# Performance work log

Measured on AMD Instinct MI355X. Metric: run time of the kernel, lower is better.

The kernel has to match this reference:

```python
import jax, jax.numpy as jnp
import numpy as np

N = 100_000   # nodes
E = 1_600_000 # edges per graph
D = 64        # feature width
HA = 32       # attention hidden


def setup_inputs() -> dict:
    key = jax.random.key(0)
    ks = jax.random.split(key, 20)
    inp = {}
    inp["h"] = jax.random.normal(ks[0], (N, D), jnp.float32)
    inp["e_od"] = jax.random.normal(ks[1], (E, D), jnp.float32)
    inp["e_ad"] = jax.random.normal(ks[2], (E, D), jnp.float32)
    inp["src_od"] = jax.random.randint(ks[3], (E,), 0, N)
    inp["dst_od"] = jax.random.randint(ks[4], (E,), 0, N)
    inp["src_ad"] = jax.random.randint(ks[5], (E,), 0, N)
    inp["dst_ad"] = jax.random.randint(ks[6], (E,), 0, N)
    s = 1.0 / np.sqrt(D).astype(np.float32)
    # stacked params: index 0 = OD graph, index 1 = AD graph
    inp["W_src"]  = jax.random.normal(ks[7],  (2, D, D), jnp.float32) * s
    inp["W_dst"]  = jax.random.normal(ks[8],  (2, D, D), jnp.float32) * s
    inp["W_edge"] = jax.random.normal(ks[9],  (2, D, D), jnp.float32) * s
    inp["b_msg"]  = jnp.zeros((2, D), jnp.float32)
    inp["W_self"] = jax.random.normal(ks[10], (2, D, D), jnp.float32) * s
    inp["W_agg"]  = jax.random.normal(ks[11], (2, D, D), jnp.float32) * s
    inp["b_node"] = jnp.zeros((2, D), jnp.float32)
    # Attention (Aggregate_samedim): Linear(D->HA, bias) -> tanh -> Linear(HA->1, no bias)
    inp["attn_l1_w"] = jax.random.normal(ks[12], (D, HA), jnp.float32) * s
    inp["attn_l1_b"] = jnp.zeros((HA,), jnp.float32)
    inp["attn_l2_w"] = jax.random.normal(ks[13], (HA, 1), jnp.float32) * (1.0 / np.sqrt(HA).astype(np.float32))
    return inp


def reference(h, e_od, e_ad, src_od, dst_od, src_ad, dst_ad,
              W_src, W_dst, W_edge, b_msg, W_self, W_agg, b_node,
              attn_l1_w, attn_l1_b, attn_l2_w):
    def mpnn(i, e, src, dst):
        # edge message: gather src/dst node feats, small GEMMs, relu  [E, D]
        m = jax.nn.relu(h[src] @ W_src[i] + h[dst] @ W_dst[i] + e @ W_edge[i] + b_msg[i])
        # scatter-sum to destination nodes  [N, D]
        agg = jax.ops.segment_sum(m, dst, num_segments=N)
        # node update  [N, D]
        return jax.nn.relu(h @ W_self[i] + agg @ W_agg[i] + b_node[i])

    intra = mpnn(0, e_od, src_od, dst_od)  # OD graph node states
    inter = mpnn(1, e_ad, src_ad, dst_ad)  # AD graph node states
    # Aggregate_samedim: attention over the 2-way stack
    rep = jnp.stack([intra, inter], axis=1)               # [N, 2, D]
    w = jnp.tanh(rep @ attn_l1_w + attn_l1_b) @ attn_l2_w  # [N, 2, 1]
    beta = jax.nn.softmax(w, axis=1)
    return (beta * rep).sum(axis=1)                        # [N, D]
```

## Files before the change

### kernel.cpp

```cpp
#include <hip/hip_runtime.h>
#include <hip/hip_bf16.h>

using short8  = __attribute__((ext_vector_type(8))) short;
using ushort8 = __attribute__((ext_vector_type(8))) unsigned short;
using f32x4   = __attribute__((ext_vector_type(4))) float;
using fvec4   = __attribute__((ext_vector_type(4))) float;

#define CH 8192

__device__ inline unsigned short f2bf(float x) {
  union { __hip_bfloat16 b; unsigned short u; } c;
  c.b = __float2bfloat16(x);
  return c.u;
}
__device__ inline float bf2f(unsigned short s) {
  return __uint_as_float(((unsigned int)s) << 16);
}
__device__ inline unsigned int pk2(float lo, float hi) {
  union { __hip_bfloat162 b; unsigned int u; } c;
  c.b = __float22bfloat162_rn(make_float2(lo, hi));
  return c.u;
}
__device__ inline short8 cvt8(fvec4 a, fvec4 b) {
  union { short8 s; unsigned int u[4]; } r;
  r.u[0] = pk2(a[0], a[1]);
  r.u[1] = pk2(a[2], a[3]);
  r.u[2] = pk2(b[0], b[1]);
  r.u[3] = pk2(b[2], b[3]);
  return r.s;
}

__device__ inline void gload_lds16(const void* g, void* l) {
  __builtin_amdgcn_global_load_lds(
      (const __attribute__((address_space(1))) void*)g,
      (__attribute__((address_space(3))) void*)l, 16, 0, 0);
}

__device__ inline void load_bfrags_f32(const float* __restrict__ W, short8 bfr[2][4], int lane) {
  int l15 = lane & 15, lh = lane >> 4;
#pragma unroll
  for (int ks = 0; ks < 2; ++ks)
#pragma unroll
    for (int ct = 0; ct < 4; ++ct) {
      short8 v;
#pragma unroll
      for (int i = 0; i < 8; ++i)
        v[i] = (short)f2bf(W[(ks * 32 + lh * 8 + i) * 64 + ct * 16 + l15]);
      bfr[ks][ct] = v;
    }
}

__device__ inline void load_bfrags(const unsigned short* __restrict__ Wf, short8 bfr[2][4], int lane) {
#pragma unroll
  for (int ks = 0; ks < 2; ++ks)
#pragma unroll
    for (int ct = 0; ct < 4; ++ct) {
      union { ushort8 u; short8 s; } c;
      c.u = *reinterpret_cast<const ushort8*>(Wf + (((ks * 4 + ct) << 9) + (lane << 3)));
      bfr[ks][ct] = c.s;
    }
}

struct PrepArgs {
  const float* W[10];
};

__global__ __launch_bounds__(64) void prep_w_kernel(PrepArgs pw, unsigned short* __restrict__ Wf) {
  int z = blockIdx.x;
  int lane = threadIdx.x & 63;
  short8 bfr[2][4];
  load_bfrags_f32(pw.W[z], bfr, lane);
  unsigned short* dst = Wf + (size_t)z * 4096;
#pragma unroll
  for (int ks = 0; ks < 2; ++ks)
#pragma unroll
    for (int ct = 0; ct < 4; ++ct) {
      union { short8 s; ushort8 u; } c;
      c.s = bfr[ks][ct];
      *reinterpret_cast<ushort8*>(dst + (((ks * 4 + ct) << 9) + (lane << 3))) = c.u;
    }
}

struct ProjArgs {
  unsigned short* out[6];
};

__global__ __launch_bounds__(256) void proj_all_kernel(const float* __restrict__ h,
                                                       const unsigned short* __restrict__ Wf,
                                                       ProjArgs pa, int N) {
  int lane = threadIdx.x & 63;
  int wv = threadIdx.x >> 6;
  int rowbase = blockIdx.x * 256 + wv * 64;
  int l15 = lane & 15, lh = lane >> 4;

  short8 afr[4][2];
#pragma unroll
  for (int rt = 0; rt < 4; ++rt) {
    int row = rowbase + rt * 16 + l15;
    int rc = row < N ? row : 0;
    const fvec4* p = reinterpret_cast<const fvec4*>(h + (size_t)rc * 64);
#pragma unroll
    for (int ks = 0; ks < 2; ++ks)
      afr[rt][ks] = cvt8(p[ks * 8 + lh * 2], p[ks * 8 + lh * 2 + 1]);
  }

  for (int z = 0; z < 6; ++z) {
    short8 bfr[2][4];
    load_bfrags(Wf + (size_t)z * 4096, bfr, lane);
    unsigned short* __restrict__ out = pa.out[z];

    f32x4 acc[4][4];
#pragma unroll
    for (int rt = 0; rt < 4; ++rt)
#pragma unroll
      for (int ct = 0; ct < 4; ++ct) acc[rt][ct] = (f32x4){0.f, 0.f, 0.f, 0.f};

#pragma unroll
    for (int rt = 0; rt < 4; ++rt)
#pragma unroll
      for (int ks = 0; ks < 2; ++ks)
#pragma unroll
        for (int ct = 0; ct < 4; ++ct)
          acc[rt][ct] = __builtin_amdgcn_mfma_f32_16x16x32_bf16(afr[rt][ks], bfr[ks][ct], acc[rt][ct], 0, 0, 0);

#pragma unroll
    for (int rt = 0; rt < 4; ++rt)
#pragma unroll
      for (int rg = 0; rg < 4; ++rg) {
        int row = rowbase + rt * 16 + lh * 4 + rg;
        if (row < N) {
#pragma unroll
          for (int ct = 0; ct < 4; ++ct)
            out[(size_t)row * 64 + ct * 16 + l15] = f2bf(acc[rt][ct][rg]);
        }
      }
  }
}

__global__ __launch_bounds__(256) void hist_kernel(const int* __restrict__ dst0, const int* __restrict__ dst1,
                                                   int* __restrict__ counts, int E, int NBK) {
  __shared__ int hcnt[2048];
  int z = blockIdx.y;
  const int* __restrict__ dst = z ? dst1 : dst0;
  int t = threadIdx.x;
  for (int i = t; i < NBK; i += 256) hcnt[i] = 0;
  __syncthreads();
  int base = blockIdx.x * CH;
#pragma unroll 4
  for (int k = 0; k < CH / 256; ++k) {
    int i = base + k * 256 + t;
    if (i < E) atomicAdd(&hcnt[dst[i] >> 6], 1);
  }
  __syncthreads();
  for (int i = t; i < NBK; i += 256) {
    int c = hcnt[i];
    if (c) atomicAdd(&counts[(size_t)z * NBK + i], c);
  }
}

__global__ __launch_bounds__(1024) void scan_kernel(const int* __restrict__ counts, int* __restrict__ cursor,
                                                    int* __restrict__ gcur, int NBK) {
  int z = blockIdx.x;
  const int* c = counts + (size_t)z * NBK;
  __shared__ int lds[1024];
  int t = threadIdx.x;
  int carry = 0;
  for (int base = 0; base < NBK; base += 1024) {
    int i = base + t;
    int v = (i < NBK) ? c[i] : 0;
    lds[t] = v;
    __syncthreads();
    for (int off = 1; off < 1024; off <<= 1) {
      int x = (t >= off) ? lds[t - off] : 0;
      __syncthreads();
      lds[t] += x;
      __syncthreads();
    }
    if (i < NBK) {
      int excl = carry + lds[t] - v;
      cursor[(size_t)z * NBK + i] = excl;
      gcur[(size_t)z * NBK + i] = excl;
    }
    carry += lds[1023];
    __syncthreads();
  }
}

__global__ __launch_bounds__(256) void scatterA_kernel(
    const int* __restrict__ src0, const int* __restrict__ dst0,
    const int* __restrict__ src1, const int* __restrict__ dst1,
    int* __restrict__ gcur, int2* __restrict__ recs0, int2* __restrict__ recs1,
    int E, int NBK) {
  __shared__ int lcnt[2048];
  int z = blockIdx.y;
  const int* __restrict__ src = z ? src1 : src0;
  const int* __restrict__ dst = z ? dst1 : dst0;
  int2* __restrict__ recs = z ? recs1 : recs0;
  int t = threadIdx.x;
  for (int i = t; i < NBK; i += 256) lcnt[i] = 0;
  __syncthreads();
  int base = blockIdx.x * CH;
#pragma unroll 4
  for (int k = 0; k < CH / 256; ++k) {
    int i = base + k * 256 + t;
    if (i < E) atomicAdd(&lcnt[dst[i] >> 6], 1);
  }
  __syncthreads();
  for (int i = t; i < NBK; i += 256) {
    int c = lcnt[i];
    lcnt[i] = c ? atomicAdd(&gcur[(size_t)z * NBK + i], c) : 0;
  }
  __syncthreads();
#pragma unroll 4
  for (int k = 0; k < CH / 256; ++k) {
    int i = base + k * 256 + t;
    if (i < E) {
      int d = dst[i], s = src[i];
      int bin = d >> 6, dl = d & 63;
      int pos = atomicAdd(&lcnt[bin], 1);
      recs[pos] = make_int2(i | (bin << 21), s | (dl << 26));
    }
  }
}

__global__ __launch_bounds__(256) void sortB_kernel(int2* __restrict__ recs0, int2* __restrict__ recs1,
                                                    const int* __restrict__ cursor,
                                                    const int* __restrict__ counts, int NBK) {
  __shared__ int cnt_lds[64];
  __shared__ int cur_lds[64];
  int z = blockIdx.y;
  int b = blockIdx.x;
  int2* __restrict__ recs = z ? recs1 : recs0;
  int start = cursor[(size_t)z * NBK + b];
  int cnt = counts[(size_t)z * NBK + b];
  int t = threadIdx.x;

  for (int cbase = 0; cbase < cnt; cbase += 2048) {
    int ccnt = min(2048, cnt - cbase);
    int2 r[8];
    int dl[8];
    if (t < 64) cnt_lds[t] = 0;
    __syncthreads();
#pragma unroll
    for (int k = 0; k < 8; ++k) {
      int idx = k * 256 + t;
      if (idx < ccnt) {
        r[k] = recs[start + cbase + idx];
        dl[k] = ((unsigned)r[k].y) >> 26;
        atomicAdd(&cnt_lds[dl[k]], 1);
      }
    }
    __syncthreads();
    if (t < 64) {
      int c = cnt_lds[t];
      int x = c;
#pragma unroll
      for (int off = 1; off < 64; off <<= 1) {
        int y = __shfl_up(x, off);
        if (t >= off) x += y;
      }
      cur_lds[t] = x - c;
    }
    __syncthreads();
#pragma unroll
    for (int k = 0; k < 8; ++k) {
      int idx = k * 256 + t;
      if (idx < ccnt) {
        int pos = atomicAdd(&cur_lds[dl[k]], 1);
        recs[start + cbase + pos] = r[k];
      }
    }
    __syncthreads();
  }
}

struct EdgeArgs {
  const float* e[2];
  const int2* recs[2];
  const unsigned short* We[2];
  const float* bmsg[2];
  const unsigned short* Ps[2];
  const unsigned short* Pd[2];
  float* agg[2];
};

__global__ __launch_bounds__(256) void edge_sorted_kernel(EdgeArgs ea, int E) {
  __shared__ float e_lds[4][64 * 64];

  int z = blockIdx.y;
  const float* __restrict__ e = ea.e[z];
  const int2* __restrict__ recs = ea.recs[z];
  const unsigned short* __restrict__ Psrc = ea.Ps[z];
  const unsigned short* __restrict__ Pdst = ea.Pd[z];
  float* __restrict__ agg = ea.agg[z];

  int lane = threadIdx.x & 63;
  int wv = threadIdx.x >> 6;
  int base = (blockIdx.x * 4 + wv) * 64;
  if (base >= E) return;
  int l15 = lane & 15, lh = lane >> 4;
  char* lbase = (char*)&e_lds[wv][0];

  int slot = base + lane;
  int el = 0, sl = 0, dl = 0;
  if (slot < E) {
    int2 rc = recs[slot];
    el = rc.x & 0x1FFFFF;
    sl = rc.y & 0x3FFFFFF;
    dl = (((rc.x >> 21) & 0x7FF) << 6) | (int)(((unsigned)rc.y) >> 26);
  }

  const float* bmsg = ea.bmsg[z];
  float bv[4];
#pragma unroll
  for (int ct = 0; ct < 4; ++ct) bv[ct] = bmsg[ct * 16 + l15];

  short8 bfr[2][4];
  load_bfrags(ea.We[z], bfr, lane);

  ushort8 aP[8], aD[8];
#pragma unroll
  for (int rt = 0; rt < 4; ++rt) {
    int sr = rt * 16 + l15;
    int hr = __shfl(sl, sr);
    int dr = __shfl(dl, sr);
    const ushort8* ps = reinterpret_cast<const ushort8*>(Psrc + ((size_t)hr << 6));
    const ushort8* pd = reinterpret_cast<const ushort8*>(Pdst + ((size_t)dr << 6));
    aP[rt * 2] = ps[lh];
    aP[rt * 2 + 1] = ps[4 + lh];
    aD[rt * 2] = pd[lh];
    aD[rt * 2 + 1] = pd[4 + lh];
  }
  __builtin_amdgcn_sched_barrier(0);

  int rgrp = lane >> 4;
#pragma unroll
  for (int i = 0; i < 16; ++i) {
    int r = i * 4 + rgrp;
    int er = __shfl(el, r);
    int c = (lane & 15) ^ (r & 7);
    gload_lds16(e + ((size_t)er << 6) + c * 4, lbase + i * 1024);
  }
  __builtin_amdgcn_sched_barrier(0);

  short8 idf[2];
#pragma unroll
  for (int half = 0; half < 2; ++half) {
    short8 v;
#pragma unroll
    for (int i = 0; i < 8; ++i)
      v[i] = (short)((lh * 8 + i == half * 16 + l15) ? 0x3F80 : 0);
    idf[half] = v;
  }

  f32x4 acc[4][4];
#pragma unroll
  for (int ct = 0; ct < 4; ++ct) {
    f32x4 bb = (f32x4){bv[ct], bv[ct], bv[ct], bv[ct]};
#pragma unroll
    for (int rt = 0; rt < 4; ++rt) acc[rt][ct] = bb;
  }

#pragma unroll
  for (int rt = 0; rt < 4; ++rt) {
    union { ushort8 u; short8 s; } aP0, aP1, aD0, aD1;
    aP0.u = aP[rt * 2];
    aP1.u = aP[rt * 2 + 1];
    aD0.u = aD[rt * 2];
    aD1.u = aD[rt * 2 + 1];
    acc[rt][0] = __builtin_amdgcn_mfma_f32_16x16x32_bf16(aP0.s, idf[0], acc[rt][0], 0, 0, 0);
    acc[rt][1] = __builtin_amdgcn_mfma_f32_16x16x32_bf16(aP0.s, idf[1], acc[rt][1], 0, 0, 0);
    acc[rt][2] = __builtin_amdgcn_mfma_f32_16x16x32_bf16(aP1.s, idf[0], acc[rt][2], 0, 0, 0);
    acc[rt][3] = __builtin_amdgcn_mfma_f32_16x16x32_bf16(aP1.s, idf[1], acc[rt][3], 0, 0, 0);
    acc[rt][0] = __builtin_amdgcn_mfma_f32_16x16x32_bf16(aD0.s, idf[0], acc[rt][0], 0, 0, 0);
    acc[rt][1] = __builtin_amdgcn_mfma_f32_16x16x32_bf16(aD0.s, idf[1], acc[rt][1], 0, 0, 0);
    acc[rt][2] = __builtin_amdgcn_mfma_f32_16x16x32_bf16(aD1.s, idf[0], acc[rt][2], 0, 0, 0);
    acc[rt][3] = __builtin_amdgcn_mfma_f32_16x16x32_bf16(aD1.s, idf[1], acc[rt][3], 0, 0, 0);
  }

  asm volatile("s_waitcnt vmcnt(0)" ::: "memory");
  __builtin_amdgcn_sched_barrier(0);

#pragma unroll
  for (int rt = 0; rt < 4; ++rt) {
    int r = rt * 16 + l15;
    int rowbyte = r << 8;
    int x = (r & 7) << 4;
    fvec4 p0 = *reinterpret_cast<const fvec4*>(lbase + rowbyte + (((lh * 2) << 4) ^ x));
    fvec4 p1 = *reinterpret_cast<const fvec4*>(lbase + rowbyte + (((lh * 2 + 1) << 4) ^ x));
    fvec4 p2 = *reinterpret_cast<const fvec4*>(lbase + rowbyte + (((8 + lh * 2) << 4) ^ x));
    fvec4 p3 = *reinterpret_cast<const fvec4*>(lbase + rowbyte + (((9 + lh * 2) << 4) ^ x));
    short8 aE0 = cvt8(p0, p1);
    short8 aE1 = cvt8(p2, p3);
#pragma unroll
    for (int ct = 0; ct < 4; ++ct) {
      acc[rt][ct] = __builtin_amdgcn_mfma_f32_16x16x32_bf16(aE0, bfr[0][ct], acc[rt][ct], 0, 0, 0);
      acc[rt][ct] = __builtin_amdgcn_mfma_f32_16x16x32_bf16(aE1, bfr[1][ct], acc[rt][ct], 0, 0, 0);
    }
  }

#pragma unroll
  for (int rt = 0; rt < 4; ++rt)
#pragma unroll
    for (int ct = 0; ct < 4; ++ct)
#pragma unroll
      for (int rg = 0; rg < 4; ++rg)
        acc[rt][ct][rg] = fmaxf(acc[rt][ct][rg], 0.f);

  int dprev = __shfl_up(dl, 1);
  unsigned long long bnd = __ballot(lane > 0 && dl != dprev);
  int vrows = min(64, E - base);

  int r0 = 0;
  while (r0 < vrows) {
    unsigned long long rest = (r0 < 63) ? (bnd >> (r0 + 1)) : 0ull;
    int r1 = rest ? (r0 + 1 + __builtin_ctzll(rest)) : 64;
    if (r1 > vrows) r1 = vrows;
    int dcur = __shfl(dl, r0);

    float s0 = 0.f, s1 = 0.f, s2 = 0.f, s3 = 0.f;
#pragma unroll
    for (int rt = 0; rt < 4; ++rt) {
      int rs = rt * 16;
      if (r0 <= rs && r1 >= rs + 16) {
#pragma unroll
        for (int rg = 0; rg < 4; ++rg) {
          s0 += acc[rt][0][rg];
          s1 += acc[rt][1][rg];
          s2 += acc[rt][2][rg];
          s3 += acc[rt][3][rg];
        }
      } else if (r0 < rs + 16 && r1 > rs) {
#pragma unroll
        for (int rg = 0; rg < 4; ++rg) {
          int row = rs + lh * 4 + rg;
          bool in = (row >= r0) && (row < r1);
          s0 += in ? acc[rt][0][rg] : 0.f;
          s1 += in ? acc[rt][1][rg] : 0.f;
          s2 += in ? acc[rt][2][rg] : 0.f;
          s3 += in ? acc[rt][3][rg] : 0.f;
        }
      }
    }
    s0 += __shfl_xor(s0, 16); s0 += __shfl_xor(s0, 32);
    s1 += __shfl_xor(s1, 16); s1 += __shfl_xor(s1, 32);
    s2 += __shfl_xor(s2, 16); s2 += __shfl_xor(s2, 32);
    s3 += __shfl_xor(s3, 16); s3 += __shfl_xor(s3, 32);
    float mine = (lh == 0) ? s0 : (lh == 1) ? s1 : (lh == 2) ? s2 : s3;
    atomicAdd(&agg[(size_t)dcur * 64 + lane], mine);
    r0 = r1;
  }
}

struct NodeArgs {
  const float* agg[2];
  const unsigned short* T[2];
  const float* bn[2];
  unsigned short* U[2];
};

__global__ __launch_bounds__(256) void node_kernel(const unsigned short* __restrict__ Wf,
                                                   NodeArgs na, int N) {
  int z = blockIdx.y;
  const float* __restrict__ agg = na.agg[z];
  const unsigned short* __restrict__ T = na.T[z];
  const float* __restrict__ bn = na.bn[z];
  unsigned short* __restrict__ U = na.U[z];
  int lane = threadIdx.x & 63;
  int wv = threadIdx.x >> 6;
  int rowbase = blockIdx.x * 256 + wv * 64;
  int l15 = lane & 15, lh = lane >> 4;

  short8 bfr[2][4];
  load_bfrags(Wf + (size_t)(8 + z) * 4096, bfr, lane);

  f32x4 acc[4][4];
#pragma unroll
  for (int rt = 0; rt < 4; ++rt)
#pragma unroll
    for (int ct = 0; ct < 4; ++ct) acc[rt][ct] = (f32x4){0.f, 0.f, 0.f, 0.f};

#pragma unroll
  for (int rt = 0; rt < 4; ++rt) {
    int row = rowbase + rt * 16 + l15;
    int rc = row < N ? row : 0;
    const fvec4* p = reinterpret_cast<const fvec4*>(agg + (size_t)rc * 64);
#pragma unroll
    for (int ks = 0; ks < 2; ++ks) {
      fvec4 p0 = p[ks * 8 + lh * 2], p1 = p[ks * 8 + lh * 2 + 1];
      short8 ahi = cvt8(p0, p1);
      fvec4 q0, q1;
#pragma unroll
      for (int i = 0; i < 4; ++i) {
        q0[i] = p0[i] - bf2f((unsigned short)ahi[i]);
        q1[i] = p1[i] - bf2f((unsigned short)ahi[i + 4]);
      }
      short8 alo = cvt8(q0, q1);
#pragma unroll
      for (int ct = 0; ct < 4; ++ct) {
        acc[rt][ct] = __builtin_amdgcn_mfma_f32_16x16x32_bf16(ahi, bfr[ks][ct], acc[rt][ct], 0, 0, 0);
        acc[rt][ct] = __builtin_amdgcn_mfma_f32_16x16x32_bf16(alo, bfr[ks][ct], acc[rt][ct], 0, 0, 0);
      }
    }
  }

  float bv[4];
#pragma unroll
  for (int ct = 0; ct < 4; ++ct) bv[ct] = bn[ct * 16 + l15];

#pragma unroll
  for (int rt = 0; rt < 4; ++rt)
#pragma unroll
    for (int rg = 0; rg < 4; ++rg) {
      int row = rowbase + rt * 16 + lh * 4 + rg;
      if (row < N) {
#pragma unroll
        for (int ct = 0; ct < 4; ++ct) {
          int c = ct * 16 + l15;
          float v = acc[rt][ct][rg] + bf2f(T[(size_t)row * 64 + c]) + bv[ct];
          U[(size_t)row * 64 + c] = f2bf(fmaxf(v, 0.0f));
        }
      }
    }
}

__global__ __launch_bounds__(256) void attn_kernel(
    const unsigned short* __restrict__ U0, const unsigned short* __restrict__ U1,
    const float* __restrict__ l1w, const float* __restrict__ l1b, const float* __restrict__ l2w,
    float* __restrict__ out, int N) {
  int t = threadIdx.x;
  int node = blockIdx.x * 64 + (t >> 2);
  int q = t & 3;
  if (node >= N) return;
  size_t b0 = (size_t)node * 64;

  float a0[8], a1[8];
#pragma unroll
  for (int i = 0; i < 8; ++i) { a0[i] = l1b[q * 8 + i]; a1[i] = a0[i]; }

  for (int k = 0; k < 64; ++k) {
    float u0 = bf2f(U0[b0 + k]);
    float u1 = bf2f(U1[b0 + k]);
#pragma unroll
    for (int i = 0; i < 8; ++i) {
      float w = l1w[k * 32 + q * 8 + i];
      a0[i] += u0 * w;
      a1[i] += u1 * w;
    }
  }
  float w0 = 0.f, w1 = 0.f;
#pragma unroll
  for (int i = 0; i < 8; ++i) {
    float l2 = l2w[q * 8 + i];
    w0 += tanhf(a0[i]) * l2;
    w1 += tanhf(a1[i]) * l2;
  }
  w0 += __shfl_xor(w0, 1, 4); w0 += __shfl_xor(w0, 2, 4);
  w1 += __shfl_xor(w1, 1, 4); w1 += __shfl_xor(w1, 2, 4);

  float m = fmaxf(w0, w1);
  float e0 = expf(w0 - m), e1 = expf(w1 - m);
  float inv = 1.0f / (e0 + e1);
  float be0 = e0 * inv, be1 = e1 * inv;

#pragma unroll
  for (int j = 0; j < 16; ++j) {
    int c = q * 16 + j;
    out[b0 + c] = be0 * bf2f(U0[b0 + c]) + be1 * bf2f(U1[b0 + c]);
  }
}

static inline size_t au(size_t x) { return (x + 255) & ~(size_t)255; }

extern "C" void kernel_launch(void* const* d_in, const int* in_sizes, int n_in,
                              void* d_out, int out_size, void* d_ws, size_t ws_size,
                              hipStream_t stream) {
  const float* h      = (const float*)d_in[0];
  const float* e_od   = (const float*)d_in[1];
  const float* e_ad   = (const float*)d_in[2];
  const int* src_od   = (const int*)d_in[3];
  const int* dst_od   = (const int*)d_in[4];
  const int* src_ad   = (const int*)d_in[5];
  const int* dst_ad   = (const int*)d_in[6];
  const float* W_src  = (const float*)d_in[7];
  const float* W_dst  = (const float*)d_in[8];
  const float* W_edge = (const float*)d_in[9];
  const float* b_msg  = (const float*)d_in[10];
  const float* W_self = (const float*)d_in[11];
  const float* W_agg  = (const float*)d_in[12];
  const float* b_node = (const float*)d_in[13];
  const float* l1w    = (const float*)d_in[14];
  const float* l1b    = (const float*)d_in[15];
  const float* l2w    = (const float*)d_in[16];
  float* out = (float*)d_out;

  int N = in_sizes[0] / 64;
  int E = in_sizes[1] / 64;
  int NBK = (N + 63) >> 6;

  char* ws = (char*)d_ws;
  size_t off = 0;
  int* counts = (int*)(ws + off);   off += au((size_t)2 * NBK * sizeof(int));
  float* agg0 = (float*)(ws + off); off += (size_t)N * 64 * sizeof(float);
  float* agg1 = (float*)(ws + off); off += (size_t)N * 64 * sizeof(float);
  size_t zero_bytes = off;
  int* cursor = (int*)(ws + off);   off += au((size_t)2 * NBK * sizeof(int));
  int* gcur   = (int*)(ws + off);   off += au((size_t)2 * NBK * sizeof(int));
  int2* recs0 = (int2*)(ws + off);  off += au((size_t)E * sizeof(int2));
  int2* recs1 = (int2*)(ws + off);  off += au((size_t)E * sizeof(int2));
  unsigned short* Wf = (unsigned short*)(ws + off); off += au((size_t)10 * 4096 * sizeof(unsigned short));
  size_t NP = au((size_t)N * 64 * sizeof(unsigned short));
  unsigned short* Psrc0 = (unsigned short*)(ws + off); off += NP;
  unsigned short* Pdst0 = (unsigned short*)(ws + off); off += NP;
  unsigned short* Psrc1 = (unsigned short*)(ws + off); off += NP;
  unsigned short* Pdst1 = (unsigned short*)(ws + off); off += NP;
  unsigned short* T0    = (unsigned short*)(ws + off); off += NP;
  unsigned short* T1    = (unsigned short*)(ws + off); off += NP;
  unsigned short* U0 = Psrc0;
  unsigned short* U1 = Psrc1;

  hipMemsetAsync(ws, 0, zero_bytes, stream);

  PrepArgs pw;
  pw.W[0] = W_src;         pw.W[1] = W_dst;
  pw.W[2] = W_src + 4096;  pw.W[3] = W_dst + 4096;
  pw.W[4] = W_self;        pw.W[5] = W_self + 4096;
  pw.W[6] = W_edge;        pw.W[7] = W_edge + 4096;
  pw.W[8] = W_agg;         pw.W[9] = W_agg + 4096;
  prep_w_kernel<<<10, 64, 0, stream>>>(pw, Wf);

  int nb = (N + 255) / 256;
  ProjArgs pa;
  pa.out[0] = Psrc0;
  pa.out[1] = Pdst0;
  pa.out[2] = Psrc1;
  pa.out[3] = Pdst1;
  pa.out[4] = T0;
  pa.out[5] = T1;
  proj_all_kernel<<<nb, 256, 0, stream>>>(h, Wf, pa, N);

  int nch = (E + CH - 1) / CH;
  hist_kernel<<<dim3(nch, 2), 256, 0, stream>>>(dst_od, dst_ad, counts, E, NBK);
  scan_kernel<<<2, 1024, 0, stream>>>(counts, cursor, gcur, NBK);
  scatterA_kernel<<<dim3(nch, 2), 256, 0, stream>>>(src_od, dst_od, src_ad, dst_ad, gcur,
                                                    recs0, recs1, E, NBK);
  sortB_kernel<<<dim3(NBK, 2), 256, 0, stream>>>(recs0, recs1, cursor, counts, NBK);

  int tiles = (E + 63) / 64;
  int eb = (tiles + 3) / 4;
  EdgeArgs ea;
  ea.e[0] = e_od;  ea.recs[0] = recs0; ea.We[0] = Wf + 6 * 4096; ea.bmsg[0] = b_msg;
  ea.Ps[0] = Psrc0; ea.Pd[0] = Pdst0; ea.agg[0] = agg0;
  ea.e[1] = e_ad;  ea.recs[1] = recs1; ea.We[1] = Wf + 7 * 4096; ea.bmsg[1] = b_msg + 64;
  ea.Ps[1] = Psrc1; ea.Pd[1] = Pdst1; ea.agg[1] = agg1;
  edge_sorted_kernel<<<dim3(eb, 2), 256, 0, stream>>>(ea, E);

  NodeArgs na;
  na.agg[0] = agg0; na.T[0] = T0; na.bn[0] = b_node;      na.U[0] = U0;
  na.agg[1] = agg1; na.T[1] = T1; na.bn[1] = b_node + 64; na.U[1] = U1;
  node_kernel<<<dim3(nb, 2), 256, 0, stream>>>(Wf, na, N);

  attn_kernel<<<(N + 63) / 64, 256, 0, stream>>>(U0, U1, l1w, l1b, l2w, out, N);
}
```

Before: 487.0 us.

## Halve edge kernel LDS via two-phase e staging; split projections across grid

The edge kernel now stages the fp32 edge-feature tile in two 32-row halves, reusing one half-size LDS buffer. It reads the first half into registers, issues async loads for the second half, and runs the first half's MFMAs while those loads are in flight. Halving LDS per block and adding launch_bounds(256,4) aims to fit more blocks per CU, at the cost of extra waits and register pressure. Separately, the six node projections are spread over a second grid dimension rather than looped in one block, which adds parallelism but re-reads and re-converts h six times.

New measurement: 603.3 us. +23.9%, slower.

```diff
diff --git a/kernel.cpp b/kernel.cpp
--- a/kernel.cpp
+++ b/kernel.cpp
@@ -88,6 +88,7 @@
 __global__ __launch_bounds__(256) void proj_all_kernel(const float* __restrict__ h,
                                                        const unsigned short* __restrict__ Wf,
                                                        ProjArgs pa, int N) {
+  int z = blockIdx.y;
   int lane = threadIdx.x & 63;
   int wv = threadIdx.x >> 6;
   int rowbase = blockIdx.x * 256 + wv * 64;
@@ -104,37 +105,35 @@
       afr[rt][ks] = cvt8(p[ks * 8 + lh * 2], p[ks * 8 + lh * 2 + 1]);
   }
 
-  for (int z = 0; z < 6; ++z) {
-    short8 bfr[2][4];
-    load_bfrags(Wf + (size_t)z * 4096, bfr, lane);
-    unsigned short* __restrict__ out = pa.out[z];
-
-    f32x4 acc[4][4];
-#pragma unroll
-    for (int rt = 0; rt < 4; ++rt)
-#pragma unroll
-      for (int ct = 0; ct < 4; ++ct) acc[rt][ct] = (f32x4){0.f, 0.f, 0.f, 0.f};
-
-#pragma unroll
-    for (int rt = 0; rt < 4; ++rt)
-#pragma unroll
-      for (int ks = 0; ks < 2; ++ks)
+  short8 bfr[2][4];
+  load_bfrags(Wf + (size_t)z * 4096, bfr, lane);
+  unsigned short* __restrict__ out = pa.out[z];
+
+  f32x4 acc[4][4];
+#pragma unroll
+  for (int rt = 0; rt < 4; ++rt)
+#pragma unroll
+    for (int ct = 0; ct < 4; ++ct) acc[rt][ct] = (f32x4){0.f, 0.f, 0.f, 0.f};
+
+#pragma unroll
+  for (int rt = 0; rt < 4; ++rt)
+#pragma unroll
+    for (int ks = 0; ks < 2; ++ks)
+#pragma unroll
+      for (int ct = 0; ct < 4; ++ct)
+        acc[rt][ct] = __builtin_amdgcn_mfma_f32_16x16x32_bf16(afr[rt][ks], bfr[ks][ct], acc[rt][ct], 0, 0, 0);
+
+#pragma unroll
+  for (int rt = 0; rt < 4; ++rt)
+#pragma unroll
+    for (int rg = 0; rg < 4; ++rg) {
+      int row = rowbase + rt * 16 + lh * 4 + rg;
+      if (row < N) {
 #pragma unroll
         for (int ct = 0; ct < 4; ++ct)
-          acc[rt][ct] = __builtin_amdgcn_mfma_f32_16x16x32_bf16(afr[rt][ks], bfr[ks][ct], acc[rt][ct], 0, 0, 0);
-
-#pragma unroll
-    for (int rt = 0; rt < 4; ++rt)
-#pragma unroll
-      for (int rg = 0; rg < 4; ++rg) {
-        int row = rowbase + rt * 16 + lh * 4 + rg;
-        if (row < N) {
-#pragma unroll
-          for (int ct = 0; ct < 4; ++ct)
-            out[(size_t)row * 64 + ct * 16 + l15] = f2bf(acc[rt][ct][rg]);
-        }
+          out[(size_t)row * 64 + ct * 16 + l15] = f2bf(acc[rt][ct][rg]);
       }
-  }
+    }
 }
 
 __global__ __launch_bounds__(256) void hist_kernel(const int* __restrict__ dst0, const int* __restrict__ dst1,
@@ -284,8 +283,8 @@
   float* agg[2];
 };
 
-__global__ __launch_bounds__(256) void edge_sorted_kernel(EdgeArgs ea, int E) {
-  __shared__ float e_lds[4][64 * 64];
+__global__ __launch_bounds__(256, 4) void edge_sorted_kernel(EdgeArgs ea, int E) {
+  __shared__ float e_lds[4][32 * 64];
 
   int z = blockIdx.y;
   const float* __restrict__ e = ea.e[z];
@@ -335,7 +334,7 @@
 
   int rgrp = lane >> 4;
 #pragma unroll
-  for (int i = 0; i < 16; ++i) {
+  for (int i = 0; i < 8; ++i) {
     int r = i * 4 + rgrp;
     int er = __shfl(el, r);
     int c = (lane & 15) ^ (r & 7);
@@ -381,11 +380,48 @@
   asm volatile("s_waitcnt vmcnt(0)" ::: "memory");
   __builtin_amdgcn_sched_barrier(0);
 
-#pragma unroll
-  for (int rt = 0; rt < 4; ++rt) {
-    int r = rt * 16 + l15;
-    int rowbyte = r << 8;
-    int x = (r & 7) << 4;
+  fvec4 h0p[2][4];
+#pragma unroll
+  for (int rt = 0; rt < 2; ++rt) {
+    int rb = rt * 16 + l15;
+    int rowbyte = rb << 8;
+    int x = (rb & 7) << 4;
+    h0p[rt][0] = *reinterpret_cast<const fvec4*>(lbase + rowbyte + (((lh * 2) << 4) ^ x));
+    h0p[rt][1] = *reinterpret_cast<const fvec4*>(lbase + rowbyte + (((lh * 2 + 1) << 4) ^ x));
+    h0p[rt][2] = *reinterpret_cast<const fvec4*>(lbase + rowbyte + (((8 + lh * 2) << 4) ^ x));
+    h0p[rt][3] = *reinterpret_cast<const fvec4*>(lbase + rowbyte + (((9 + lh * 2) << 4) ^ x));
+  }
+  asm volatile("s_waitcnt lgkmcnt(0)" ::: "memory");
+  __builtin_amdgcn_sched_barrier(0);
+
+#pragma unroll
+  for (int i = 0; i < 8; ++i) {
+    int rb = i * 4 + rgrp;
+    int er = __shfl(el, 32 + rb);
+    int c = (lane & 15) ^ (rb & 7);
+    gload_lds16(e + ((size_t)er << 6) + c * 4, lbase + i * 1024);
+  }
+  __builtin_amdgcn_sched_barrier(0);
+
+#pragma unroll
+  for (int rt = 0; rt < 2; ++rt) {
+    short8 aE0 = cvt8(h0p[rt][0], h0p[rt][1]);
+    short8 aE1 = cvt8(h0p[rt][2], h0p[rt][3]);
+#pragma unroll
+    for (int ct = 0; ct < 4; ++ct) {
+      acc[rt][ct] = __builtin_amdgcn_mfma_f32_16x16x32_bf16(aE0, bfr[0][ct], acc[rt][ct], 0, 0, 0);
+      acc[rt][ct] = __builtin_amdgcn_mfma_f32_16x16x32_bf16(aE1, bfr[1][ct], acc[rt][ct], 0, 0, 0);
+    }
+  }
+
+  asm volatile("s_waitcnt vmcnt(0)" ::: "memory");
+  __builtin_amdgcn_sched_barrier(0);
+
+#pragma unroll
+  for (int rt = 2; rt < 4; ++rt) {
+    int rb = (rt - 2) * 16 + l15;
+    int rowbyte = rb << 8;
+    int x = (rb & 7) << 4;
     fvec4 p0 = *reinterpret_cast<const fvec4*>(lbase + rowbyte + (((lh * 2) << 4) ^ x));
     fvec4 p1 = *reinterpret_cast<const fvec4*>(lbase + rowbyte + (((lh * 2 + 1) << 4) ^ x));
     fvec4 p2 = *reinterpret_cast<const fvec4*>(lbase + rowbyte + (((8 + lh * 2) << 4) ^ x));
@@ -637,7 +673,7 @@
   pa.out[3] = Pdst1;
   pa.out[4] = T0;
   pa.out[5] = T1;
-  proj_all_kernel<<<nb, 256, 0, stream>>>(h, Wf, pa, N);
+  proj_all_kernel<<<dim3(nb, 6), 256, 0, stream>>>(h, Wf, pa, N);
 
   int nch = (E + CH - 1) / CH;
   hist_kernel<<<dim3(nch, 2), 256, 0, stream>>>(dst_od, dst_ad, counts, E, NBK);
```
